# Kernel tuning notes

Measured on AMD Instinct MI355X. Metric: run time of the kernel, lower is better.

The kernel has to match this reference:

```python
import jax, jax.numpy as jnp
from jax import lax
import numpy as np

MS = 128            # local_map_size
HALF = MS // 2
B, S = 8, 64
C, H, W = 3, 1024, 1024


def setup_inputs() -> dict:
    key = jax.random.key(0)
    ks = jax.random.split(key, 48)
    r = lambda i, shape, s: jax.random.normal(ks[i], shape, jnp.float32) * s
    z = lambda *shape: jnp.zeros(shape, jnp.float32)
    o = lambda *shape: jnp.ones(shape, jnp.float32)
    return {
        "full_map": jax.random.normal(ks[0], (B, C, H, W), jnp.float32),
        "conditions": jax.random.uniform(ks[1], (B, 5), jnp.float32, 0.0, 1024.0),
        "input_seq": jax.random.uniform(ks[2], (B, S, 2), jnp.float32, 0.0, 1024.0),
        "steps_remaining": jax.random.uniform(ks[3], (B, S), jnp.float32, 0.0, 500.0),
        # LocalMapEncoder convs (OIHW) + batchnorm affine params
        "cw1": r(4, (16, 3, 3, 3), 0.2),   "cb1": z(16),  "g1": o(16),  "be1": z(16),
        "cw2": r(5, (32, 16, 3, 3), 0.1),  "cb2": z(32),  "g2": o(32),  "be2": z(32),
        "cw3": r(6, (64, 32, 3, 3), 0.07), "cb3": z(64),  "g3": o(64),  "be3": z(64),
        "cw4": r(7, (128, 64, 3, 3), 0.05),"cb4": z(128), "g4": o(128), "be4": z(128),
        "fw1": r(8, (512, 128 * 8 * 8), 0.01), "fb1": z(512),
        "fw2": r(9, (256, 512), 0.04),         "fb2": z(256),
        # ConditionEncoder (6 -> 128 -> 64)
        "ew1": r(10, (128, 6), 0.05),  "eb1": z(128),
        "ew2": r(11, (64, 128), 0.05), "eb2": z(64),
        # coord embedder (2 -> 32)
        "mw": r(12, (32, 2), 0.05), "mb": z(32),
        # 2-layer LSTM, torch gate order (i, f, g, o)
        "w_ih0": r(13, (4 * 256, 32), 0.05),  "w_hh0": r(14, (4 * 256, 256), 0.05),
        "b_ih0": z(4 * 256), "b_hh0": z(4 * 256),
        "w_ih1": r(15, (4 * 256, 256), 0.05), "w_hh1": r(16, (4 * 256, 256), 0.05),
        "b_ih1": z(4 * 256), "b_hh1": z(4 * 256),
        # context layer (256+256+64=576 -> 128 -> 64) and output (64 -> 2)
        "xw1": r(17, (128, 576), 0.04), "xb1": z(128),
        "xw2": r(18, (64, 128), 0.05),  "xb2": z(64),
        "ow": r(19, (2, 64), 0.1),      "ob": z(2),
    }


def _conv_bn_relu(x, w, b, g, be):
    # stride-2 3x3 conv, padding 1, NCHW/OIHW; BatchNorm in training mode (batch stats)
    y = lax.conv_general_dilated(x, w, (2, 2), ((1, 1), (1, 1)),
                                 dimension_numbers=("NCHW", "OIHW", "NCHW"))
    y = y + b[None, :, None, None]
    mu = y.mean((0, 2, 3), keepdims=True)
    var = y.var((0, 2, 3), keepdims=True)
    y = (y - mu) * lax.rsqrt(var + 1e-5) * g[None, :, None, None] + be[None, :, None, None]
    return jax.nn.relu(y)


def _lstm_layer(x, w_ih, w_hh, b_ih, b_hh):
    # x: [B, S, D] -> hidden states [B, S, Hd]
    bsz, hd = x.shape[0], w_hh.shape[1]
    bias = b_ih + b_hh
    def step(carry, xt):
        h, c = carry
        zg = xt @ w_ih.T + h @ w_hh.T + bias
        i, f, gg, oo = jnp.split(zg, 4, axis=-1)
        c = jax.nn.sigmoid(f) * c + jax.nn.sigmoid(i) * jnp.tanh(gg)
        h = jax.nn.sigmoid(oo) * jnp.tanh(c)
        return (h, c), h
    h0 = jnp.zeros((bsz, hd), x.dtype)
    _, hs = lax.scan(step, (h0, h0), x.transpose(1, 0, 2))
    return hs.transpose(1, 0, 2)


def reference(full_map, conditions, input_seq, steps_remaining,
              cw1, cb1, g1, be1, cw2, cb2, g2, be2,
              cw3, cb3, g3, be3, cw4, cb4, g4, be4,
              fw1, fb1, fw2, fb2, ew1, eb1, ew2, eb2, mw, mb,
              w_ih0, w_hh0, b_ih0, b_hh0, w_ih1, w_hh1, b_ih1, b_hh1,
              xw1, xb1, xw2, xb2, ow, ob):
    bsz, seq, _ = input_seq.shape
    # --- batched crop+pad gather (replaces host numpy loop): zero-pad map by
    # HALF on each side, then every crop is a dynamic_slice of size MS at (y, x).
    padded = jnp.pad(full_map, ((0, 0), (0, 0), (HALF, HALF), (HALF, HALF)))
    ys = input_seq[..., 0].astype(jnp.int32).reshape(-1)
    xs = input_seq[..., 1].astype(jnp.int32).reshape(-1)
    bidx = jnp.repeat(jnp.arange(bsz, dtype=jnp.int32), seq)
    crop_one = lambda b, y, x: lax.dynamic_slice(padded, (b, 0, y, x), (1, C, MS, MS))[0]
    crops = jax.vmap(crop_one)(bidx, ys, xs)              # [B*S, C, MS, MS]
    # --- LocalMapEncoder
    h = _conv_bn_relu(crops, cw1, cb1, g1, be1)
    h = _conv_bn_relu(h, cw2, cb2, g2, be2)
    h = _conv_bn_relu(h, cw3, cb3, g3, be3)
    h = _conv_bn_relu(h, cw4, cb4, g4, be4)               # [B*S, 128, 8, 8]
    h = h.reshape(h.shape[0], -1)
    h = jax.nn.relu(h @ fw1.T + fb1) @ fw2.T + fb2
    map_features = h.reshape(bsz, seq, -1)                # [B, S, 256]
    # --- ConditionEncoder on [conditions ++ steps_remaining]
    enh = jnp.concatenate(
        [jnp.broadcast_to(conditions[:, None, :], (bsz, seq, 5)),
         steps_remaining[..., None]], axis=-1)            # [B, S, 6]
    cond_features = jax.nn.relu(enh @ ew1.T + eb1) @ ew2.T + eb2  # [B, S, 64]
    # --- route predictor
    emb = jax.nn.relu(input_seq @ mw.T + mb)              # [B, S, 32]
    lstm_out = _lstm_layer(emb, w_ih0, w_hh0, b_ih0, b_hh0)
    lstm_out = _lstm_layer(lstm_out, w_ih1, w_hh1, b_ih1, b_hh1)  # [B, S, 256]
    combined = jnp.concatenate([lstm_out, map_features, cond_features], axis=-1)
    ctx = jax.nn.relu(jax.nn.relu(combined @ xw1.T + xb1) @ xw2.T + xb2)
    return ctx @ ow.T + ob                                # [B, S, 2]
```

## Files before the change

kernel.cpp:

```cpp
#include <hip/hip_runtime.h>

#define TPB 256
#define NLB 64

typedef float f32x4 __attribute__((ext_vector_type(4)));
typedef short bf16x8 __attribute__((ext_vector_type(8)));
typedef unsigned long long u64;

__device__ __forceinline__ float bf2f(unsigned short u) {
  union { unsigned int i; float f; } x; x.i = ((unsigned int)u) << 16; return x.f;
}
__device__ __forceinline__ unsigned short f2bf(float v) {
  union { float f; unsigned int i; } x; x.f = v;
  unsigned int r = (x.i + 0x7fffu + ((x.i >> 16) & 1u)) >> 16;
  return (unsigned short)r;
}
__device__ __forceinline__ float sigf(float x) { return 1.f / (1.f + __expf(-x)); }
__device__ __forceinline__ bf16x8 lda_bf8(const unsigned short* p) {
  union { uint4 u; bf16x8 v; } t; t.u = *(const uint4*)p; return t.v;
}
__device__ __forceinline__ float fma8(uint4 q, const float* w, float a) {
  union { unsigned int u; float f; } t;
  t.u = q.x << 16;         a = fmaf(w[0], t.f, a);
  t.u = q.x & 0xffff0000u; a = fmaf(w[1], t.f, a);
  t.u = q.y << 16;         a = fmaf(w[2], t.f, a);
  t.u = q.y & 0xffff0000u; a = fmaf(w[3], t.f, a);
  t.u = q.z << 16;         a = fmaf(w[4], t.f, a);
  t.u = q.z & 0xffff0000u; a = fmaf(w[5], t.f, a);
  t.u = q.w << 16;         a = fmaf(w[6], t.f, a);
  t.u = q.w & 0xffff0000u; a = fmaf(w[7], t.f, a);
  return a;
}

__global__ __launch_bounds__(TPB, 2) void conv1_tap(
    const float* __restrict__ fmap, const float* __restrict__ iseq,
    const unsigned short* __restrict__ wT,
    const float* __restrict__ bias,
    unsigned short* __restrict__ out) {
  __shared__ float patch[3][17][132];
  __shared__ unsigned short Bsm[16][104];
  __shared__ float bs[16];
  const int tid = threadIdx.x;
  const int n = blockIdx.x >> 3, R0 = (blockIdx.x & 7) << 3;
  const int y = (int)iseq[n * 2], x = (int)iseq[n * 2 + 1];
  const int bimg = n >> 6;

  for (int e = tid; e < 1536; e += TPB) Bsm[e / 96][e % 96] = wT[e];
  if (tid < 16) bs[tid] = bias[tid];
  for (int e = tid; e < 3 * 17 * 132; e += TPB) {
    int ic = e / 2244, rem = e % 2244, l = rem / 132, c = rem % 132;
    int i = 2 * R0 - 1 + l, j = c - 1;
    float v = 0.f;
    if ((unsigned)i < 128u && (unsigned)j < 128u) {
      int r = y + i - 64, cc = x + j - 64;
      if ((unsigned)r < 1024u && (unsigned)cc < 1024u)
        v = fmap[(((size_t)bimg * 3 + ic) << 20) + ((size_t)r << 10) + cc];
    }
    patch[ic][l][c] = v;
  }
  __syncthreads();

  const int w = tid >> 6, lane = tid & 63, fr = lane & 15, kg = lane >> 4;
  f32x4 acc[8];
#pragma unroll
  for (int m = 0; m < 8; ++m) acc[m] = {0.f, 0.f, 0.f, 0.f};

#pragma unroll
  for (int ch = 0; ch < 3; ++ch) {
    int k8 = ch * 4 + kg;
    int ki = (k8 >= 9) ? 0 : ((k8 * 11) >> 5);
    int kj = (k8 >= 9) ? 0 : (k8 - 3 * ki);
    bf16x8 bfr = lda_bf8(&Bsm[fr][k8 * 8]);
#pragma unroll
    for (int m = 0; m < 8; ++m) {
      int p = w * 128 + m * 16 + fr;
      int pr = p >> 6, pc = p & 63;
      int l = 2 * pr + ki, c = 2 * pc + kj;
      bf16x8 af = {(short)f2bf(patch[0][l][c]), (short)f2bf(patch[1][l][c]),
                   (short)f2bf(patch[2][l][c]), 0, 0, 0, 0, 0};
      acc[m] = __builtin_amdgcn_mfma_f32_16x16x32_bf16(af, bfr, acc[m], 0, 0, 0);
    }
  }
  const int rg = lane >> 4;
  float bb = bs[fr];
#pragma unroll
  for (int m = 0; m < 8; ++m) {
#pragma unroll
    for (int r = 0; r < 4; ++r) {
      int p = w * 128 + m * 16 + rg * 4 + r;
      int pr = p >> 6, pc = p & 63;
      out[(((size_t)n * 64 + R0 + pr) * 64 + pc) * 16 + fr] = f2bf(acc[m][r] + bb);
    }
  }
}

template<int CIN, int COUT_BLK, int NSPLIT, int HIN, int HOUT>
__global__ __launch_bounds__(TPB, 2) void conv_tap(
    const unsigned short* __restrict__ inb,
    const float* __restrict__ ss,
    const unsigned short* __restrict__ wT,
    const float* __restrict__ bias,
    unsigned short* __restrict__ out) {
  constexpr int K = CIN * 9;
  constexpr int K8 = K / 8;
  constexpr int NCH = (K8 + 3) / 4;
  constexpr int KPAD = NCH * 32;
  constexpr int BS = KPAD + 8;
  constexpr int CINP = CIN + 8;
  constexpr int ICG_SH = (CIN == 16) ? 1 : (CIN == 32) ? 2 : 3;
  constexpr int TPR = HOUT / 8;
  constexpr int TILES = TPR * TPR;
  constexpr int NT = COUT_BLK / 16;
  constexpr int COUT_TOT = COUT_BLK * NSPLIT;

  __shared__ unsigned short patch[289 * CINP];
  __shared__ unsigned short Bsm[COUT_BLK * BS];
  __shared__ float ssl[CIN * 2];

  const int tid = threadIdx.x;
  const int bid = blockIdx.x;
  const int n = bid / (TILES * NSPLIT);
  const int rem = bid % (TILES * NSPLIT);
  const int tile = rem / NSPLIT;
  const int split = rem % NSPLIT;
  const int TR0 = (tile / TPR) * 8, TC0 = (tile % TPR) * 8;
  const int oc0 = split * COUT_BLK;

  for (int i = tid; i < CIN * 2; i += TPB) ssl[i] = ss[i];
  __syncthreads();

  for (int e = tid; e < 289 * (CIN / 8); e += TPB) {
    int icg = e % (CIN / 8), pix = e / (CIN / 8);
    int row = pix / 17, col = pix % 17;
    int ir = 2 * TR0 - 1 + row, jc = 2 * TC0 - 1 + col;
    uint4 o = {0u, 0u, 0u, 0u};
    if ((unsigned)ir < (unsigned)HIN && (unsigned)jc < (unsigned)HIN) {
      uint4 v = *(const uint4*)&inb[(((size_t)n * HIN + ir) * HIN + jc) * CIN + icg * 8];
      unsigned int d[4] = {v.x, v.y, v.z, v.w};
      unsigned int* op = (unsigned int*)&o;
#pragma unroll
      for (int t = 0; t < 4; ++t) {
        int c = icg * 8 + 2 * t;
        float a = fmaxf(fmaf(bf2f((unsigned short)(d[t] & 0xffff)), ssl[2 * c], ssl[2 * c + 1]), 0.f);
        float b = fmaxf(fmaf(bf2f((unsigned short)(d[t] >> 16)), ssl[2 * c + 2], ssl[2 * c + 3]), 0.f);
        op[t] = (unsigned int)f2bf(a) | ((unsigned int)f2bf(b) << 16);
      }
    }
    *(uint4*)&patch[pix * CINP + icg * 8] = o;
  }
  constexpr int B8 = COUT_BLK * (KPAD / 8);
  for (int e = tid; e < B8; e += TPB) {
    int oc = e / (KPAD / 8), k8i = e % (KPAD / 8);
    uint4 v = {0u, 0u, 0u, 0u};
    if (k8i * 8 < K) v = *(const uint4*)&wT[(size_t)(oc0 + oc) * K + k8i * 8];
    *(uint4*)&Bsm[oc * BS + k8i * 8] = v;
  }
  __syncthreads();

  const int wave = tid >> 6, lane = tid & 63;
  const int fr = lane & 15, kg = lane >> 4;
  const int p = wave * 16 + fr;
  const int pr = p >> 3, pc = p & 7;
  f32x4 acc[NT];
#pragma unroll
  for (int j = 0; j < NT; ++j) acc[j] = {0.f, 0.f, 0.f, 0.f};

#pragma unroll
  for (int ch = 0; ch < NCH; ++ch) {
    int k8 = ch * 4 + kg;
    int tap = k8 >> ICG_SH, icg = k8 & ((1 << ICG_SH) - 1);
    int ki = (tap * 11) >> 5;
    int kj = tap - 3 * ki;
    int addr = ((2 * pr + ki) * 17 + (2 * pc + kj)) * CINP + icg * 8;
    if (tap >= 9) addr = 0;
    bf16x8 af = lda_bf8(&patch[addr]);
#pragma unroll
    for (int j = 0; j < NT; ++j) {
      bf16x8 bfr = lda_bf8(&Bsm[(j * 16 + fr) * BS + ch * 32 + kg * 8]);
      acc[j] = __builtin_amdgcn_mfma_f32_16x16x32_bf16(af, bfr, acc[j], 0, 0, 0);
    }
  }
  const int rg = lane >> 4;
#pragma unroll
  for (int j = 0; j < NT; ++j) {
    int oc = oc0 + j * 16 + fr;
    float bb = bias[oc];
#pragma unroll
    for (int r = 0; r < 4; ++r) {
      int pp = wave * 16 + rg * 4 + r;
      int orow = TR0 + (pp >> 3), ocol = TC0 + (pp & 7);
      out[(((size_t)n * HOUT + orow) * HOUT + ocol) * COUT_TOT + oc] = f2bf(acc[j][r] + bb);
    }
  }
}

__global__ __launch_bounds__(TPB) void prep_wt(
    const float* __restrict__ w1, const float* __restrict__ w2,
    const float* __restrict__ w3, const float* __restrict__ w4,
    unsigned short* __restrict__ wt1, unsigned short* __restrict__ wt2,
    unsigned short* __restrict__ wt3, unsigned short* __restrict__ wt4) {
  int i = blockIdx.x * TPB + threadIdx.x;
  if (i < 1536) {
    int oc = i / 96, k = i % 96;
    int tap = k >> 3, ic = k & 7;
    float v = (tap < 9 && ic < 3) ? w1[(oc * 3 + ic) * 9 + tap] : 0.f;
    wt1[i] = f2bf(v);
  } else if (i < 6144) {
    int j = i - 1536;
    int oc = j / 144, k = j % 144;
    wt2[j] = f2bf(w2[(oc * 16 + (k & 15)) * 9 + (k >> 4)]);
  } else if (i < 24576) {
    int j = i - 6144;
    int oc = j / 288, k = j % 288;
    wt3[j] = f2bf(w3[(oc * 32 + (k & 31)) * 9 + (k >> 5)]);
  } else if (i < 98304) {
    int j = i - 24576;
    int oc = j / 576, k = j % 576;
    wt4[j] = f2bf(w4[(oc * 64 + (k & 63)) * 9 + (k >> 6)]);
  }
}

__global__ __launch_bounds__(TPB) void permute_fw1(const float* __restrict__ in,
    unsigned short* __restrict__ out) {
  __shared__ unsigned short l[128 * 66];
  int n = blockIdx.x;
  for (int e = threadIdx.x; e < 8192; e += TPB) {
    int c = e >> 6, pix = e & 63;
    l[c * 66 + pix] = f2bf(in[(size_t)n * 8192 + e]);
  }
  __syncthreads();
  for (int e = threadIdx.x; e < 8192; e += TPB) {
    int pix = e >> 7, c = e & 127;
    out[(size_t)n * 8192 + e] = l[c * 66 + pix];
  }
}

#define STAT_NB 512
__global__ __launch_bounds__(TPB) void stats_cl2(
    const unsigned short* __restrict__ y, float* __restrict__ part,
    int C, int total_u4) {
  const int tid = threadIdx.x, bid = blockIdx.x;
  const int NQ = C >> 3;
  float s[8], q[8];
#pragma unroll
  for (int j = 0; j < 8; ++j) { s[j] = 0.f; q[j] = 0.f; }
  for (int i = bid * TPB + tid; i < total_u4; i += STAT_NB * TPB) {
    uint4 v = ((const uint4*)y)[i];
    unsigned int d[4] = {v.x, v.y, v.z, v.w};
#pragma unroll
    for (int t = 0; t < 4; ++t) {
      float a = bf2f((unsigned short)(d[t] & 0xffff));
      float b = bf2f((unsigned short)(d[t] >> 16));
      s[2 * t] += a;     q[2 * t] = fmaf(a, a, q[2 * t]);
      s[2 * t + 1] += b; q[2 * t + 1] = fmaf(b, b, q[2 * t + 1]);
    }
  }
  __shared__ float rs[TPB][8];
  __shared__ float rq[TPB][8];
#pragma unroll
  for (int j = 0; j < 8; ++j) { rs[tid][j] = s[j]; rq[tid][j] = q[j]; }
  __syncthreads();
  for (int off = TPB / 2; off >= NQ; off >>= 1) {
    if (tid < off) {
#pragma unroll
      for (int j = 0; j < 8; ++j) { rs[tid][j] += rs[tid + off][j]; rq[tid][j] += rq[tid + off][j]; }
    }
    __syncthreads();
  }
  if (tid < NQ) {
#pragma unroll
    for (int j = 0; j < 8; ++j) {
      int c = tid * 8 + j;
      part[(size_t)bid * 2 * C + 2 * c] = rs[tid][j];
      part[(size_t)bid * 2 * C + 2 * c + 1] = rq[tid][j];
    }
  }
}

__global__ __launch_bounds__(TPB) void stats_final2(const float* __restrict__ part,
    const float* __restrict__ gamma, const float* __restrict__ beta,
    float* __restrict__ ss, float inv_count, int C) {
  int c = blockIdx.x, tid = threadIdx.x;
  float sum = part[(size_t)tid * 2 * C + 2 * c] + part[(size_t)(tid + 256) * 2 * C + 2 * c];
  float sq  = part[(size_t)tid * 2 * C + 2 * c + 1] + part[(size_t)(tid + 256) * 2 * C + 2 * c + 1];
  __shared__ float rs[TPB], rq[TPB];
  rs[tid] = sum; rq[tid] = sq;
  __syncthreads();
  for (int off = TPB / 2; off > 0; off >>= 1) {
    if (tid < off) { rs[tid] += rs[tid + off]; rq[tid] += rq[tid + off]; }
    __syncthreads();
  }
  if (tid == 0) {
    float mean = rs[0] * inv_count;
    float var  = rq[0] * inv_count - mean * mean;
    float rstd = rsqrtf(var + 1e-5f);
    float scl  = gamma[c] * rstd;
    ss[2 * c] = scl;
    ss[2 * c + 1] = beta[c] - mean * scl;
  }
}

__global__ __launch_bounds__(TPB) void bnrelu_cl(const unsigned short* __restrict__ y,
    const float* __restrict__ ss, unsigned short* __restrict__ out) {
  int q = blockIdx.x * TPB + threadIdx.x;
  if (q >= 524288) return;
  int c0 = (q << 3) & 127;
  uint4 v = ((const uint4*)y)[q];
  unsigned int d[4] = {v.x, v.y, v.z, v.w};
  uint4 o;
  unsigned int* op = (unsigned int*)&o;
#pragma unroll
  for (int t = 0; t < 4; ++t) {
    int c = c0 + 2 * t;
    float a = fmaxf(fmaf(bf2f((unsigned short)(d[t] & 0xffff)), ss[2 * c], ss[2 * c + 1]), 0.f);
    float b = fmaxf(fmaf(bf2f((unsigned short)(d[t] >> 16)), ss[2 * c + 2], ss[2 * c + 3]), 0.f);
    op[t] = (unsigned int)f2bf(a) | ((unsigned int)f2bf(b) << 16);
  }
  ((uint4*)out)[q] = o;
}

__global__ __launch_bounds__(TPB, 2) void fc1_mfma(
    const unsigned short* __restrict__ A, const unsigned short* __restrict__ W,
    const float* __restrict__ bias, float* __restrict__ out) {
  __shared__ unsigned short As[64][64];
  __shared__ unsigned short Bs[64][64];
  const int tid = threadIdx.x;
  const int lane = tid & 63, wave = tid >> 6;
  const int wr = (wave >> 1) * 32, wc = (wave & 1) * 32;
  const int bm = blockIdx.y * 64, bn = blockIdx.x * 64;
  f32x4 acc00 = {0.f, 0.f, 0.f, 0.f}, acc01 = acc00, acc10 = acc00, acc11 = acc00;
  const int r0 = tid >> 3, c0 = tid & 7;
  const int fr = lane & 15, kg = lane >> 4;
  for (int kt = 0; kt < 128; ++kt) {
    const int kb = kt * 64;
    uint4 av0 = *(const uint4*)&A[(size_t)(bm + r0) * 8192 + kb + c0 * 8];
    uint4 av1 = *(const uint4*)&A[(size_t)(bm + r0 + 32) * 8192 + kb + c0 * 8];
    uint4 bv0 = *(const uint4*)&W[(size_t)(bn + r0) * 8192 + kb + c0 * 8];
    uint4 bv1 = *(const uint4*)&W[(size_t)(bn + r0 + 32) * 8192 + kb + c0 * 8];
    __syncthreads();
    *(uint4*)&As[r0][(c0 ^ (r0 & 7)) * 8] = av0;
    *(uint4*)&As[r0 + 32][(c0 ^ (r0 & 7)) * 8] = av1;
    *(uint4*)&Bs[r0][(c0 ^ (r0 & 7)) * 8] = bv0;
    *(uint4*)&Bs[r0 + 32][(c0 ^ (r0 & 7)) * 8] = bv1;
    __syncthreads();
#pragma unroll
    for (int ks = 0; ks < 2; ++ks) {
      int ch = ks * 4 + kg;
      int ra0 = wr + fr, ra1 = wr + 16 + fr;
      int rb0 = wc + fr, rb1 = wc + 16 + fr;
      bf16x8 a_0 = lda_bf8(&As[ra0][(ch ^ (ra0 & 7)) * 8]);
      bf16x8 a_1 = lda_bf8(&As[ra1][(ch ^ (ra1 & 7)) * 8]);
      bf16x8 b_0 = lda_bf8(&Bs[rb0][(ch ^ (rb0 & 7)) * 8]);
      bf16x8 b_1 = lda_bf8(&Bs[rb1][(ch ^ (rb1 & 7)) * 8]);
      acc00 = __builtin_amdgcn_mfma_f32_16x16x32_bf16(a_0, b_0, acc00, 0, 0, 0);
      acc01 = __builtin_amdgcn_mfma_f32_16x16x32_bf16(a_0, b_1, acc01, 0, 0, 0);
      acc10 = __builtin_amdgcn_mfma_f32_16x16x32_bf16(a_1, b_0, acc10, 0, 0, 0);
      acc11 = __builtin_amdgcn_mfma_f32_16x16x32_bf16(a_1, b_1, acc11, 0, 0, 0);
    }
  }
  const int rg = lane >> 4;
  int n0 = bn + wc + fr, n1 = n0 + 16;
  float bi0 = bias[n0], bi1 = bias[n1];
#pragma unroll
  for (int r = 0; r < 4; ++r) {
    int m0 = bm + wr + rg * 4 + r, m1 = m0 + 16;
    out[m0 * 512 + n0] = fmaxf(acc00[r] + bi0, 0.f);
    out[m0 * 512 + n1] = fmaxf(acc01[r] + bi1, 0.f);
    out[m1 * 512 + n0] = fmaxf(acc10[r] + bi0, 0.f);
    out[m1 * 512 + n1] = fmaxf(acc11[r] + bi1, 0.f);
  }
}

__global__ __launch_bounds__(TPB, 2) void gemm_m64(
    const float* __restrict__ A, const float* __restrict__ W,
    const float* __restrict__ bias, float* __restrict__ out,
    int N, int K, int relu, int ldo, int coff) {
  __shared__ unsigned short As[64 * 40];
  __shared__ unsigned short Bs[64 * 40];
  const int tid = threadIdx.x, lane = tid & 63, wave = tid >> 6;
  const int wr = (wave >> 1) * 32, wc = (wave & 1) * 32;
  const int bm = blockIdx.y * 64, bn = blockIdx.x * 64;
  const int fr = lane & 15, kg = lane >> 4;
  const int sr = tid >> 2, sc = (tid & 3) * 8;
  f32x4 a00 = {0.f, 0.f, 0.f, 0.f}, a01 = a00, a10 = a00, a11 = a00;
  int nch = (K + 31) >> 5;
  for (int ch = 0; ch < nch; ++ch) {
    int kb = ch * 32;
    __syncthreads();
    {
      unsigned short tmp[8];
#pragma unroll
      for (int j = 0; j < 8; ++j) {
        int k = kb + sc + j;
        tmp[j] = (k < K) ? f2bf(A[(size_t)(bm + sr) * K + k]) : (unsigned short)0;
      }
      *(uint4*)&As[sr * 40 + sc] = *(const uint4*)tmp;
      int wrow = bn + sr;
#pragma unroll
      for (int j = 0; j < 8; ++j) {
        int k = kb + sc + j;
        tmp[j] = (wrow < N && k < K) ? f2bf(W[(size_t)wrow * K + k]) : (unsigned short)0;
      }
      *(uint4*)&Bs[sr * 40 + sc] = *(const uint4*)tmp;
    }
    __syncthreads();
    bf16x8 af0 = lda_bf8(&As[(wr + fr) * 40 + kg * 8]);
    bf16x8 af1 = lda_bf8(&As[(wr + 16 + fr) * 40 + kg * 8]);
    bf16x8 bf0 = lda_bf8(&Bs[(wc + fr) * 40 + kg * 8]);
    bf16x8 bf1 = lda_bf8(&Bs[(wc + 16 + fr) * 40 + kg * 8]);
    a00 = __builtin_amdgcn_mfma_f32_16x16x32_bf16(af0, bf0, a00, 0, 0, 0);
    a01 = __builtin_amdgcn_mfma_f32_16x16x32_bf16(af0, bf1, a01, 0, 0, 0);
    a10 = __builtin_amdgcn_mfma_f32_16x16x32_bf16(af1, bf0, a10, 0, 0, 0);
    a11 = __builtin_amdgcn_mfma_f32_16x16x32_bf16(af1, bf1, a11, 0, 0, 0);
  }
  const int rg = lane >> 4;
  int n0 = bn + wc + fr, n1 = n0 + 16;
  float bi0 = (n0 < N) ? bias[n0] : 0.f;
  float bi1 = (n1 < N) ? bias[n1] : 0.f;
#pragma unroll
  for (int r = 0; r < 4; ++r) {
    int m0 = bm + wr + rg * 4 + r, m1 = m0 + 16;
    if (n0 < N) {
      float v = a00[r] + bi0; out[(size_t)m0 * ldo + coff + n0] = relu ? fmaxf(v, 0.f) : v;
      v = a10[r] + bi0;       out[(size_t)m1 * ldo + coff + n0] = relu ? fmaxf(v, 0.f) : v;
    }
    if (n1 < N) {
      float v = a01[r] + bi1; out[(size_t)m0 * ldo + coff + n1] = relu ? fmaxf(v, 0.f) : v;
      v = a11[r] + bi1;       out[(size_t)m1 * ldo + coff + n1] = relu ? fmaxf(v, 0.f) : v;
    }
  }
}

__global__ __launch_bounds__(TPB) void build_enh_kernel(const float* __restrict__ cond,
    const float* __restrict__ steps, float* __restrict__ enh) {
  int i = blockIdx.x * TPB + threadIdx.x;
  if (i >= 512 * 6) return;
  int n = i / 6, k = i % 6;
  int b = n >> 6, s = n & 63;
  enh[i] = (k < 5) ? cond[b * 5 + k] : steps[b * 64 + s];
}

__global__ __launch_bounds__(TPB, 1) void lstm_kernel(
    const float* __restrict__ iseq,
    const float* __restrict__ mw, const float* __restrict__ mb,
    const float* __restrict__ w_ih0, const float* __restrict__ w_hh0,
    const float* __restrict__ b_ih0, const float* __restrict__ b_hh0,
    const float* __restrict__ w_ih1, const float* __restrict__ w_hh1,
    const float* __restrict__ b_ih1, const float* __restrict__ b_hh1,
    u64* __restrict__ h0x, u64* __restrict__ h1x,
    float* __restrict__ comb) {
  const int tid = threadIdx.x;
  const int blkid = blockIdx.x;
  const int u0 = blkid * 4;

  __shared__ float xz[64][8][16];
  __shared__ __align__(16) char reg2[26112];
  __shared__ float bias1s[16];

  float (*embc)[8][32] = (float (*)[8][32])reg2;
  float* mwmb = (float*)(reg2 + 16384);
  unsigned short (*v0s)[256] = (unsigned short (*)[256])reg2;
  unsigned short (*w1h)[256] = (unsigned short (*)[256])(reg2 + 4096);
  float (*part0)[8][16] = (float (*)[8][16])(reg2 + 8192);
  float (*part1)[8][16] = (float (*)[8][16])(reg2 + 16384);
  float (*zg0)[16] = (float (*)[16])(reg2 + 24576);
  float (*zg1)[16] = (float (*)[16])(reg2 + 25088);

  const int r = tid & 15, ks = tid >> 4;
  const int R = (r >> 2) * 256 + u0 + (r & 3);

  float w0reg[16], w1reg[32], wtmp[32];
#pragma unroll
  for (int i = 0; i < 16; ++i) w0reg[i] = w_hh0[R * 256 + ks * 16 + i];
  if (ks < 8) {
#pragma unroll
    for (int i = 0; i < 32; ++i) w1reg[i] = w_ih1[R * 256 + ks * 32 + i];
  } else {
#pragma unroll
    for (int i = 0; i < 32; ++i) w1reg[i] = w_hh1[R * 256 + (ks - 8) * 32 + i];
  }
#pragma unroll
  for (int i = 0; i < 32; ++i) wtmp[i] = w_ih0[R * 32 + i];
  const float bias0r = b_ih0[R] + b_hh0[R];
  if (tid < 16) bias1s[tid] = b_ih1[R] + b_hh1[R];
  if (tid < 96) mwmb[tid] = (tid < 64) ? mw[tid] : mb[tid - 64];
  __syncthreads();

  for (int chunk = 0; chunk < 4; ++chunk) {
    if (tid < 128) {
      int pp = tid >> 3, b = tid & 7;
      int pg = chunk * 16 + pp;
      float s0 = iseq[(b * 64 + pg) * 2 + 0];
      float s1 = iseq[(b * 64 + pg) * 2 + 1];
      for (int k = 0; k < 32; ++k)
        embc[pp][b][k] = fmaxf(fmaf(mwmb[2 * k], s0, fmaf(mwmb[2 * k + 1], s1, mwmb[64 + k])), 0.f);
    }
    __syncthreads();
    {
      int pg = chunk * 16 + ks;
      for (int b = 0; b < 8; ++b) {
        float a = bias0r;
        const float* e = &embc[ks][b][0];
#pragma unroll
        for (int k = 0; k < 32; ++k) a = fmaf(wtmp[k], e[k], a);
        xz[pg][b][r] = a;
      }
    }
    __syncthreads();
  }

  float c0 = 0.f, c1 = 0.f;
  for (int p = 0; p <= 64; ++p) {
    if (p >= 1) {
      const unsigned tag0 = (unsigned)p;
      const u64* s0p = &h0x[(size_t)(p - 1) * 1024 + tid * 4];
      u64 a0, a1, a2, a3;
      for (;;) {
        a0 = __hip_atomic_load(&s0p[0], __ATOMIC_RELAXED, __HIP_MEMORY_SCOPE_AGENT);
        a1 = __hip_atomic_load(&s0p[1], __ATOMIC_RELAXED, __HIP_MEMORY_SCOPE_AGENT);
        a2 = __hip_atomic_load(&s0p[2], __ATOMIC_RELAXED, __HIP_MEMORY_SCOPE_AGENT);
        a3 = __hip_atomic_load(&s0p[3], __ATOMIC_RELAXED, __HIP_MEMORY_SCOPE_AGENT);
        if (((unsigned)(a0 >> 32) == tag0) & ((unsigned)(a1 >> 32) == tag0) &
            ((unsigned)(a2 >> 32) == tag0) & ((unsigned)(a3 >> 32) == tag0)) break;
        __builtin_amdgcn_s_sleep(1);
      }
#pragma unroll
      for (int i = 0; i < 4; ++i) {
        int g = tid * 4 + i;
        int bb = (g & 15) >> 1, ub = (g >> 4) * 4 + (g & 1) * 2;
        u64 va = (i == 0) ? a0 : (i == 1) ? a1 : (i == 2) ? a2 : a3;
        *(unsigned int*)&v0s[bb][ub] = (unsigned int)va;
      }
    } else {
#pragma unroll
      for (int i = 0; i < 4; ++i) ((unsigned int*)v0s)[tid * 4 + i] = 0u;
    }
    __syncthreads();

    if (p < 64) {
#pragma unroll
      for (int b = 0; b < 8; ++b) {
        uint4 q0 = *(const uint4*)&v0s[b][ks * 16];
        uint4 q1 = *(const uint4*)&v0s[b][ks * 16 + 8];
        float a = 0.f;
        a = fma8(q0, &w0reg[0], a);
        a = fma8(q1, &w0reg[8], a);
        part0[ks][b][r] = a;
      }
    }
    __syncthreads();

    if (tid < 128) {
      if (p < 64) {
        int b = tid >> 4, rr = tid & 15;
        float s = xz[p][b][rr];
#pragma unroll
        for (int k2 = 0; k2 < 16; ++k2) s += part0[k2][b][rr];
        zg0[b][rr] = s;
      }
    } else {
      int t2 = tid - 128;
      if (p >= 2) {
        const unsigned tag1 = (unsigned)(p - 1);
        const u64* s1p = &h1x[(size_t)(p - 2) * 1024 + t2 * 8];
        u64 e[8];
        for (;;) {
          bool ok = true;
#pragma unroll
          for (int i = 0; i < 8; ++i) {
            e[i] = __hip_atomic_load(&s1p[i], __ATOMIC_RELAXED, __HIP_MEMORY_SCOPE_AGENT);
            ok &= ((unsigned)(e[i] >> 32) == tag1);
          }
          if (ok) break;
          __builtin_amdgcn_s_sleep(1);
        }
#pragma unroll
        for (int i = 0; i < 8; ++i) {
          int g = t2 * 8 + i;
          int bb = (g & 15) >> 1, ub = (g >> 4) * 4 + (g & 1) * 2;
          *(unsigned int*)&w1h[bb][ub] = (unsigned int)e[i];
        }
      } else {
#pragma unroll
        for (int i = 0; i < 8; ++i) ((unsigned int*)w1h)[t2 * 8 + i] = 0u;
      }
    }
    __syncthreads();

    if (tid < 32 && p < 64) {
      int b = tid >> 2, uu = tid & 3;
      float zi = zg0[b][uu], zf = zg0[b][4 + uu], zgv = zg0[b][8 + uu], zo = zg0[b][12 + uu];
      c0 = sigf(zf) * c0 + sigf(zi) * tanhf(zgv);
      float h = sigf(zo) * tanhf(c0);
      float hp = __shfl_xor(h, 1);
      if (!(uu & 1)) {
        unsigned int d = (unsigned int)f2bf(h) | ((unsigned int)f2bf(hp) << 16);
        u64 v = ((u64)(unsigned)(p + 1) << 32) | d;
        __hip_atomic_store(&h0x[(size_t)p * 1024 + blkid * 16 + b * 2 + (uu >> 1)], v,
                           __ATOMIC_RELAXED, __HIP_MEMORY_SCOPE_AGENT);
      }
    }

    if (p >= 1) {
      const unsigned short* sp = (ks < 8) ? &v0s[0][ks * 32] : &w1h[0][(ks - 8) * 32];
#pragma unroll
      for (int b = 0; b < 8; ++b) {
        const uint4* qp = (const uint4*)(sp + b * 256);
        float a = 0.f;
        a = fma8(qp[0], &w1reg[0], a);
        a = fma8(qp[1], &w1reg[8], a);
        a = fma8(qp[2], &w1reg[16], a);
        a = fma8(qp[3], &w1reg[24], a);
        part1[ks][b][r] = a;
      }
    }
    __syncthreads();

    if (tid >= 128 && p >= 1) {
      int t2 = tid - 128, b = t2 >> 4, rr = t2 & 15;
      float s = bias1s[rr];
#pragma unroll
      for (int k2 = 0; k2 < 16; ++k2) s += part1[k2][b][rr];
      zg1[b][rr] = s;
    }
    __syncthreads();

    if (tid < 32 && p >= 1) {
      int b = tid >> 2, uu = tid & 3;
      float zi = zg1[b][uu], zf = zg1[b][4 + uu], zgv = zg1[b][8 + uu], zo = zg1[b][12 + uu];
      c1 = sigf(zf) * c1 + sigf(zi) * tanhf(zgv);
      float h = sigf(zo) * tanhf(c1);
      comb[(size_t)(b * 64 + (p - 1)) * 576 + u0 + uu] = h;
      float hp = __shfl_xor(h, 1);
      if (!(uu & 1)) {
        unsigned int d = (unsigned int)f2bf(h) | ((unsigned int)f2bf(hp) << 16);
        u64 v = ((u64)(unsigned)p << 32) | d;
        __hip_atomic_store(&h1x[(size_t)(p - 1) * 1024 + blkid * 16 + b * 2 + (uu >> 1)], v,
                           __ATOMIC_RELAXED, __HIP_MEMORY_SCOPE_AGENT);
      }
    }
  }
}

extern "C" void kernel_launch(void* const* d_in, const int* in_sizes, int n_in,
                              void* d_out, int out_size, void* d_ws, size_t ws_size,
                              hipStream_t stream) {
  const float* fmap  = (const float*)d_in[0];
  const float* cond  = (const float*)d_in[1];
  const float* iseq  = (const float*)d_in[2];
  const float* steps = (const float*)d_in[3];
  const float* cw1 = (const float*)d_in[4];  const float* cb1 = (const float*)d_in[5];
  const float* g1  = (const float*)d_in[6];  const float* be1 = (const float*)d_in[7];
  const float* cw2 = (const float*)d_in[8];  const float* cb2 = (const float*)d_in[9];
  const float* g2  = (const float*)d_in[10]; const float* be2 = (const float*)d_in[11];
  const float* cw3 = (const float*)d_in[12]; const float* cb3 = (const float*)d_in[13];
  const float* g3  = (const float*)d_in[14]; const float* be3 = (const float*)d_in[15];
  const float* cw4 = (const float*)d_in[16]; const float* cb4 = (const float*)d_in[17];
  const float* g4  = (const float*)d_in[18]; const float* be4 = (const float*)d_in[19];
  const float* fw1 = (const float*)d_in[20]; const float* fb1 = (const float*)d_in[21];
  const float* fw2 = (const float*)d_in[22]; const float* fb2 = (const float*)d_in[23];
  const float* ew1 = (const float*)d_in[24]; const float* eb1 = (const float*)d_in[25];
  const float* ew2 = (const float*)d_in[26]; const float* eb2 = (const float*)d_in[27];
  const float* mw  = (const float*)d_in[28]; const float* mb  = (const float*)d_in[29];
  const float* w_ih0 = (const float*)d_in[30]; const float* w_hh0 = (const float*)d_in[31];
  const float* b_ih0 = (const float*)d_in[32]; const float* b_hh0 = (const float*)d_in[33];
  const float* w_ih1 = (const float*)d_in[34]; const float* w_hh1 = (const float*)d_in[35];
  const float* b_ih1 = (const float*)d_in[36]; const float* b_hh1 = (const float*)d_in[37];
  const float* xw1 = (const float*)d_in[38]; const float* xb1 = (const float*)d_in[39];
  const float* xw2 = (const float*)d_in[40]; const float* xb2 = (const float*)d_in[41];
  const float* ow  = (const float*)d_in[42]; const float* ob  = (const float*)d_in[43];

  float* ws = (float*)d_ws;
  unsigned short* y1bf  = (unsigned short*)ws;
  unsigned short* y2bf  = (unsigned short*)(ws + 16777216);
  unsigned short* y3bf  = (unsigned short*)(ws + 25165824);
  unsigned short* y4pre = (unsigned short*)(ws + 29360128);
  unsigned short* y4bn  = (unsigned short*)(ws + 31457280);
  unsigned short* fw1bf = (unsigned short*)(ws + 33554432);
  size_t base = 35651584;
  float* part  = ws + base; base += 131072;
  float* ss1   = ws + base; base += 32;
  float* ss2   = ws + base; base += 64;
  float* ss3   = ws + base; base += 128;
  float* ss4   = ws + base; base += 256;
  float* f1    = ws + base; base += 262144;
  float* enh   = ws + base; base += 3072;
  float* ceh   = ws + base; base += 65536;
  u64*   h0x   = (u64*)(ws + base); base += 131072;
  u64*   h1x   = (u64*)(ws + base); base += 131072;
  float* comb  = ws + base; base += 294912;
  float* cx1   = ws + base; base += 65536;
  float* cx2   = ws + base; base += 32768;
  unsigned short* wt1 = (unsigned short*)(ws + base); base += 768;
  unsigned short* wt2 = (unsigned short*)(ws + base); base += 2304;
  unsigned short* wt3 = (unsigned short*)(ws + base); base += 9216;
  unsigned short* wt4 = (unsigned short*)(ws + base); base += 36864;

  prep_wt<<<384, TPB, 0, stream>>>(cw1, cw2, cw3, cw4, wt1, wt2, wt3, wt4);
  permute_fw1<<<512, TPB, 0, stream>>>(fw1, fw1bf);

  conv1_tap<<<4096, TPB, 0, stream>>>(fmap, iseq, wt1, cb1, y1bf);
  stats_cl2<<<STAT_NB, TPB, 0, stream>>>(y1bf, part, 16, 4194304);
  stats_final2<<<16, TPB, 0, stream>>>(part, g1, be1, ss1, 1.f / 2097152.f, 16);
  conv_tap<16, 32, 1, 64, 32><<<8192, TPB, 0, stream>>>(y1bf, ss1, wt2, cb2, y2bf);
  stats_cl2<<<STAT_NB, TPB, 0, stream>>>(y2bf, part, 32, 2097152);
  stats_final2<<<32, TPB, 0, stream>>>(part, g2, be2, ss2, 1.f / 524288.f, 32);
  conv_tap<32, 64, 1, 32, 16><<<2048, TPB, 0, stream>>>(y2bf, ss2, wt3, cb3, y3bf);
  stats_cl2<<<STAT_NB, TPB, 0, stream>>>(y3bf, part, 64, 1048576);
  stats_final2<<<64, TPB, 0, stream>>>(part, g3, be3, ss3, 1.f / 131072.f, 64);
  conv_tap<64, 32, 4, 16, 8><<<2048, TPB, 0, stream>>>(y3bf, ss3, wt4, cb4, y4pre);
  stats_cl2<<<STAT_NB, TPB, 0, stream>>>(y4pre, part, 128, 524288);
  stats_final2<<<128, TPB, 0, stream>>>(part, g4, be4, ss4, 1.f / 32768.f, 128);
  bnrelu_cl<<<2048, TPB, 0, stream>>>(y4pre, ss4, y4bn);

  hipMemsetAsync(h0x, 0, 2 * 64 * 1024 * sizeof(u64), stream);
  lstm_kernel<<<NLB, TPB, 0, stream>>>(iseq, mw, mb,
                                       w_ih0, w_hh0, b_ih0, b_hh0,
                                       w_ih1, w_hh1, b_ih1, b_hh1,
                                       h0x, h1x, comb);

  fc1_mfma<<<dim3(8, 8), TPB, 0, stream>>>(y4bn, fw1bf, fb1, f1);
  gemm_m64<<<dim3(4, 8), TPB, 0, stream>>>(f1, fw2, fb2, comb, 256, 512, 0, 576, 256);

  build_enh_kernel<<<12, TPB, 0, stream>>>(cond, steps, enh);
  gemm_m64<<<dim3(2, 8), TPB, 0, stream>>>(enh, ew1, eb1, ceh, 128, 6, 1, 128, 0);
  gemm_m64<<<dim3(1, 8), TPB, 0, stream>>>(ceh, ew2, eb2, comb, 64, 128, 0, 576, 512);

  gemm_m64<<<dim3(2, 8), TPB, 0, stream>>>(comb, xw1, xb1, cx1, 128, 576, 1, 128, 0);
  gemm_m64<<<dim3(1, 8), TPB, 0, stream>>>(cx1, xw2, xb2, cx2, 64, 128, 1, 64, 0);
  gemm_m64<<<dim3(1, 8), TPB, 0, stream>>>(cx2, ow, ob, (float*)d_out, 2, 64, 0, 2, 0);
}
```

Before: 673.6 us.

## Use MFMA for LSTM recurrences, fuse BN-ReLU into fc1, bf16 channel-interleaved conv1 patch

The LSTM recurrent matvecs drop their scalar FMA partial-sum reductions. Weights are now held as bf16 MFMA fragments, one wave each for w_hh0, w_ih1 and w_hh1, which cuts the number of barriers per timestep. The final BatchNorm+ReLU is applied on the fly while fc1 loads its A tile, which removes a separate kernel and an intermediate buffer. conv1 now stores its input patch as bf16 with the channels interleaved, so each fragment is a single 16-byte LDS load instead of three float reads and conversions. The cost is bf16 rounding of the LSTM weights and recurrent state, which lowers precision.

```diff
diff --git a/kernel.cpp b/kernel.cpp
--- a/kernel.cpp
+++ b/kernel.cpp
@@ -19,17 +19,9 @@
 __device__ __forceinline__ bf16x8 lda_bf8(const unsigned short* p) {
   union { uint4 u; bf16x8 v; } t; t.u = *(const uint4*)p; return t.v;
 }
-__device__ __forceinline__ float fma8(uint4 q, const float* w, float a) {
-  union { unsigned int u; float f; } t;
-  t.u = q.x << 16;         a = fmaf(w[0], t.f, a);
-  t.u = q.x & 0xffff0000u; a = fmaf(w[1], t.f, a);
-  t.u = q.y << 16;         a = fmaf(w[2], t.f, a);
-  t.u = q.y & 0xffff0000u; a = fmaf(w[3], t.f, a);
-  t.u = q.z << 16;         a = fmaf(w[4], t.f, a);
-  t.u = q.z & 0xffff0000u; a = fmaf(w[5], t.f, a);
-  t.u = q.w << 16;         a = fmaf(w[6], t.f, a);
-  t.u = q.w & 0xffff0000u; a = fmaf(w[7], t.f, a);
-  return a;
+__device__ __forceinline__ bf16x8 frag_of(const unsigned int* w) {
+  union { unsigned int u[4]; bf16x8 v; } t;
+  t.u[0] = w[0]; t.u[1] = w[1]; t.u[2] = w[2]; t.u[3] = w[3]; return t.v;
 }
 
 __global__ __launch_bounds__(TPB, 2) void conv1_tap(
@@ -37,7 +29,7 @@
     const unsigned short* __restrict__ wT,
     const float* __restrict__ bias,
     unsigned short* __restrict__ out) {
-  __shared__ float patch[3][17][132];
+  __shared__ __align__(16) unsigned short patch[17][132][8];
   __shared__ unsigned short Bsm[16][104];
   __shared__ float bs[16];
   const int tid = threadIdx.x;
@@ -47,6 +39,9 @@
 
   for (int e = tid; e < 1536; e += TPB) Bsm[e / 96][e % 96] = wT[e];
   if (tid < 16) bs[tid] = bias[tid];
+  for (int e = tid; e < 17 * 132; e += TPB)
+    *(uint4*)&patch[e / 132][e % 132][0] = uint4{0u, 0u, 0u, 0u};
+  __syncthreads();
   for (int e = tid; e < 3 * 17 * 132; e += TPB) {
     int ic = e / 2244, rem = e % 2244, l = rem / 132, c = rem % 132;
     int i = 2 * R0 - 1 + l, j = c - 1;
@@ -56,7 +51,7 @@
       if ((unsigned)r < 1024u && (unsigned)cc < 1024u)
         v = fmap[(((size_t)bimg * 3 + ic) << 20) + ((size_t)r << 10) + cc];
     }
-    patch[ic][l][c] = v;
+    patch[l][c][ic] = f2bf(v);
   }
   __syncthreads();
 
@@ -75,9 +70,7 @@
     for (int m = 0; m < 8; ++m) {
       int p = w * 128 + m * 16 + fr;
       int pr = p >> 6, pc = p & 63;
-      int l = 2 * pr + ki, c = 2 * pc + kj;
-      bf16x8 af = {(short)f2bf(patch[0][l][c]), (short)f2bf(patch[1][l][c]),
-                   (short)f2bf(patch[2][l][c]), 0, 0, 0, 0, 0};
+      bf16x8 af = lda_bf8(&patch[2 * pr + ki][2 * pc + kj][0]);
       acc[m] = __builtin_amdgcn_mfma_f32_16x16x32_bf16(af, bfr, acc[m], 0, 0, 0);
     }
   }
@@ -300,30 +293,25 @@
   }
 }
 
-__global__ __launch_bounds__(TPB) void bnrelu_cl(const unsigned short* __restrict__ y,
-    const float* __restrict__ ss, unsigned short* __restrict__ out) {
-  int q = blockIdx.x * TPB + threadIdx.x;
-  if (q >= 524288) return;
-  int c0 = (q << 3) & 127;
-  uint4 v = ((const uint4*)y)[q];
+__device__ __forceinline__ uint4 bnpack(uint4 v, const float* sst) {
   unsigned int d[4] = {v.x, v.y, v.z, v.w};
-  uint4 o;
-  unsigned int* op = (unsigned int*)&o;
+  uint4 o; unsigned int* op = (unsigned int*)&o;
 #pragma unroll
   for (int t = 0; t < 4; ++t) {
-    int c = c0 + 2 * t;
-    float a = fmaxf(fmaf(bf2f((unsigned short)(d[t] & 0xffff)), ss[2 * c], ss[2 * c + 1]), 0.f);
-    float b = fmaxf(fmaf(bf2f((unsigned short)(d[t] >> 16)), ss[2 * c + 2], ss[2 * c + 3]), 0.f);
+    float a = fmaxf(fmaf(bf2f((unsigned short)(d[t] & 0xffff)), sst[4 * t], sst[4 * t + 1]), 0.f);
+    float b = fmaxf(fmaf(bf2f((unsigned short)(d[t] >> 16)), sst[4 * t + 2], sst[4 * t + 3]), 0.f);
     op[t] = (unsigned int)f2bf(a) | ((unsigned int)f2bf(b) << 16);
   }
-  ((uint4*)out)[q] = o;
+  return o;
 }
 
 __global__ __launch_bounds__(TPB, 2) void fc1_mfma(
     const unsigned short* __restrict__ A, const unsigned short* __restrict__ W,
-    const float* __restrict__ bias, float* __restrict__ out) {
+    const float* __restrict__ ss, const float* __restrict__ bias,
+    float* __restrict__ out) {
   __shared__ unsigned short As[64][64];
   __shared__ unsigned short Bs[64][64];
+  __shared__ float ssl[256];
   const int tid = threadIdx.x;
   const int lane = tid & 63, wave = tid >> 6;
   const int wr = (wave >> 1) * 32, wc = (wave & 1) * 32;
@@ -331,13 +319,18 @@
   f32x4 acc00 = {0.f, 0.f, 0.f, 0.f}, acc01 = acc00, acc10 = acc00, acc11 = acc00;
   const int r0 = tid >> 3, c0 = tid & 7;
   const int fr = lane & 15, kg = lane >> 4;
+  for (int i = tid; i < 256; i += TPB) ssl[i] = ss[i];
+  __syncthreads();
   for (int kt = 0; kt < 128; ++kt) {
     const int kb = kt * 64;
     uint4 av0 = *(const uint4*)&A[(size_t)(bm + r0) * 8192 + kb + c0 * 8];
     uint4 av1 = *(const uint4*)&A[(size_t)(bm + r0 + 32) * 8192 + kb + c0 * 8];
     uint4 bv0 = *(const uint4*)&W[(size_t)(bn + r0) * 8192 + kb + c0 * 8];
     uint4 bv1 = *(const uint4*)&W[(size_t)(bn + r0 + 32) * 8192 + kb + c0 * 8];
-    __syncthreads();
+    const float* sst = &ssl[2 * ((kb + c0 * 8) & 127)];
+    __syncthreads();
+    av0 = bnpack(av0, sst);
+    av1 = bnpack(av1, sst);
     *(uint4*)&As[r0][(c0 ^ (r0 & 7)) * 8] = av0;
     *(uint4*)&As[r0 + 32][(c0 ^ (r0 & 7)) * 8] = av1;
     *(uint4*)&Bs[r0][(c0 ^ (r0 & 7)) * 8] = bv0;
@@ -454,31 +447,35 @@
   const int u0 = blkid * 4;
 
   __shared__ float xz[64][8][16];
-  __shared__ __align__(16) char reg2[26112];
+  __shared__ __align__(16) char reg2[18944];
   __shared__ float bias1s[16];
 
   float (*embc)[8][32] = (float (*)[8][32])reg2;
   float* mwmb = (float*)(reg2 + 16384);
-  unsigned short (*v0s)[256] = (unsigned short (*)[256])reg2;
-  unsigned short (*w1h)[256] = (unsigned short (*)[256])(reg2 + 4096);
-  float (*part0)[8][16] = (float (*)[8][16])(reg2 + 8192);
-  float (*part1)[8][16] = (float (*)[8][16])(reg2 + 16384);
-  float (*zg0)[16] = (float (*)[16])(reg2 + 24576);
-  float (*zg1)[16] = (float (*)[16])(reg2 + 25088);
-
+  unsigned short (*v0s)[264] = (unsigned short (*)[264])reg2;
+  unsigned short (*w1h)[264] = (unsigned short (*)[264])(reg2 + 8448);
+  float (*P0)[16]  = (float (*)[16])(reg2 + 16896);
+  float (*P1a)[16] = (float (*)[16])(reg2 + 17408);
+  float (*P1b)[16] = (float (*)[16])(reg2 + 17920);
+
+  const int wv = tid >> 6, lane = tid & 63, fr = lane & 15, kg = lane >> 4;
   const int r = tid & 15, ks = tid >> 4;
-  const int R = (r >> 2) * 256 + u0 + (r & 3);
-
-  float w0reg[16], w1reg[32], wtmp[32];
-#pragma unroll
-  for (int i = 0; i < 16; ++i) w0reg[i] = w_hh0[R * 256 + ks * 16 + i];
-  if (ks < 8) {
-#pragma unroll
-    for (int i = 0; i < 32; ++i) w1reg[i] = w_ih1[R * 256 + ks * 32 + i];
-  } else {
-#pragma unroll
-    for (int i = 0; i < 32; ++i) w1reg[i] = w_hh1[R * 256 + (ks - 8) * 32 + i];
-  }
+  const int R  = (r >> 2) * 256 + u0 + (r & 3);
+  const int Rf = (fr >> 2) * 256 + u0 + (fr & 3);
+
+  unsigned int wfrag[8][4];
+  {
+    const float* wsrc = (wv == 0) ? w_hh0 : (wv == 1) ? w_ih1 : w_hh1;
+#pragma unroll
+    for (int ch = 0; ch < 8; ++ch)
+#pragma unroll
+      for (int d = 0; d < 4; ++d) {
+        float lo = wsrc[(size_t)Rf * 256 + ch * 32 + kg * 8 + d * 2];
+        float hi = wsrc[(size_t)Rf * 256 + ch * 32 + kg * 8 + d * 2 + 1];
+        wfrag[ch][d] = (unsigned)f2bf(lo) | ((unsigned)f2bf(hi) << 16);
+      }
+  }
+  float wtmp[32];
 #pragma unroll
   for (int i = 0; i < 32; ++i) wtmp[i] = w_ih0[R * 32 + i];
   const float bias0r = b_ih0[R] + b_hh0[R];
@@ -509,54 +506,42 @@
     __syncthreads();
   }
 
+  for (int i = tid; i < 8 * 264; i += TPB) {
+    v0s[8 + i / 264][i % 264] = 0;
+    w1h[8 + i / 264][i % 264] = 0;
+  }
+  __syncthreads();
+
   float c0 = 0.f, c1 = 0.f;
   for (int p = 0; p <= 64; ++p) {
-    if (p >= 1) {
-      const unsigned tag0 = (unsigned)p;
-      const u64* s0p = &h0x[(size_t)(p - 1) * 1024 + tid * 4];
-      u64 a0, a1, a2, a3;
-      for (;;) {
-        a0 = __hip_atomic_load(&s0p[0], __ATOMIC_RELAXED, __HIP_MEMORY_SCOPE_AGENT);
-        a1 = __hip_atomic_load(&s0p[1], __ATOMIC_RELAXED, __HIP_MEMORY_SCOPE_AGENT);
-        a2 = __hip_atomic_load(&s0p[2], __ATOMIC_RELAXED, __HIP_MEMORY_SCOPE_AGENT);
-        a3 = __hip_atomic_load(&s0p[3], __ATOMIC_RELAXED, __HIP_MEMORY_SCOPE_AGENT);
-        if (((unsigned)(a0 >> 32) == tag0) & ((unsigned)(a1 >> 32) == tag0) &
-            ((unsigned)(a2 >> 32) == tag0) & ((unsigned)(a3 >> 32) == tag0)) break;
-        __builtin_amdgcn_s_sleep(1);
-      }
-#pragma unroll
-      for (int i = 0; i < 4; ++i) {
-        int g = tid * 4 + i;
-        int bb = (g & 15) >> 1, ub = (g >> 4) * 4 + (g & 1) * 2;
-        u64 va = (i == 0) ? a0 : (i == 1) ? a1 : (i == 2) ? a2 : a3;
-        *(unsigned int*)&v0s[bb][ub] = (unsigned int)va;
-      }
-    } else {
-#pragma unroll
-      for (int i = 0; i < 4; ++i) ((unsigned int*)v0s)[tid * 4 + i] = 0u;
-    }
-    __syncthreads();
-
-    if (p < 64) {
-#pragma unroll
-      for (int b = 0; b < 8; ++b) {
-        uint4 q0 = *(const uint4*)&v0s[b][ks * 16];
-        uint4 q1 = *(const uint4*)&v0s[b][ks * 16 + 8];
-        float a = 0.f;
-        a = fma8(q0, &w0reg[0], a);
-        a = fma8(q1, &w0reg[8], a);
-        part0[ks][b][r] = a;
-      }
-    }
-    __syncthreads();
-
     if (tid < 128) {
-      if (p < 64) {
-        int b = tid >> 4, rr = tid & 15;
-        float s = xz[p][b][rr];
-#pragma unroll
-        for (int k2 = 0; k2 < 16; ++k2) s += part0[k2][b][rr];
-        zg0[b][rr] = s;
+      if (p >= 1) {
+        const unsigned tag0 = (unsigned)p;
+        const u64* s0p = &h0x[(size_t)(p - 1) * 1024 + tid * 8];
+        u64 e[8];
+        for (;;) {
+          bool ok = true;
+#pragma unroll
+          for (int i = 0; i < 8; ++i) {
+            e[i] = __hip_atomic_load(&s0p[i], __ATOMIC_RELAXED, __HIP_MEMORY_SCOPE_AGENT);
+            ok &= ((unsigned)(e[i] >> 32) == tag0);
+          }
+          if (ok) break;
+          __builtin_amdgcn_s_sleep(1);
+        }
+#pragma unroll
+        for (int i = 0; i < 8; ++i) {
+          int g = tid * 8 + i;
+          int bb = (g >> 1) & 7, ub = (g >> 4) * 4 + (g & 1) * 2;
+          *(unsigned int*)&v0s[bb][ub] = (unsigned int)e[i];
+        }
+      } else {
+#pragma unroll
+        for (int i = 0; i < 8; ++i) {
+          int g = tid * 8 + i;
+          int bb = (g >> 1) & 7, ub = (g >> 4) * 4 + (g & 1) * 2;
+          *(unsigned int*)&v0s[bb][ub] = 0u;
+        }
       }
     } else {
       int t2 = tid - 128;
@@ -577,20 +562,72 @@
 #pragma unroll
         for (int i = 0; i < 8; ++i) {
           int g = t2 * 8 + i;
-          int bb = (g & 15) >> 1, ub = (g >> 4) * 4 + (g & 1) * 2;
+          int bb = (g >> 1) & 7, ub = (g >> 4) * 4 + (g & 1) * 2;
           *(unsigned int*)&w1h[bb][ub] = (unsigned int)e[i];
         }
       } else {
 #pragma unroll
-        for (int i = 0; i < 8; ++i) ((unsigned int*)w1h)[t2 * 8 + i] = 0u;
+        for (int i = 0; i < 8; ++i) {
+          int g = t2 * 8 + i;
+          int bb = (g >> 1) & 7, ub = (g >> 4) * 4 + (g & 1) * 2;
+          *(unsigned int*)&w1h[bb][ub] = 0u;
+        }
+      }
+    }
+    __syncthreads();
+
+    if (wv == 0) {
+      if (p < 64) {
+        f32x4 acc = {0.f, 0.f, 0.f, 0.f};
+#pragma unroll
+        for (int ch = 0; ch < 8; ++ch) {
+          bf16x8 af = lda_bf8(&v0s[fr][ch * 32 + kg * 8]);
+          acc = __builtin_amdgcn_mfma_f32_16x16x32_bf16(af, frag_of(wfrag[ch]), acc, 0, 0, 0);
+        }
+#pragma unroll
+        for (int j = 0; j < 4; ++j) {
+          int bb2 = (lane >> 4) * 4 + j;
+          if (bb2 < 8) P0[bb2][fr] = acc[j];
+        }
+      }
+    } else if (wv == 1) {
+      if (p >= 1) {
+        f32x4 acc = {0.f, 0.f, 0.f, 0.f};
+#pragma unroll
+        for (int ch = 0; ch < 8; ++ch) {
+          bf16x8 af = lda_bf8(&v0s[fr][ch * 32 + kg * 8]);
+          acc = __builtin_amdgcn_mfma_f32_16x16x32_bf16(af, frag_of(wfrag[ch]), acc, 0, 0, 0);
+        }
+#pragma unroll
+        for (int j = 0; j < 4; ++j) {
+          int bb2 = (lane >> 4) * 4 + j;
+          if (bb2 < 8) P1a[bb2][fr] = acc[j];
+        }
+      }
+    } else if (wv == 2) {
+      if (p >= 1) {
+        f32x4 acc = {0.f, 0.f, 0.f, 0.f};
+#pragma unroll
+        for (int ch = 0; ch < 8; ++ch) {
+          bf16x8 af = lda_bf8(&w1h[fr][ch * 32 + kg * 8]);
+          acc = __builtin_amdgcn_mfma_f32_16x16x32_bf16(af, frag_of(wfrag[ch]), acc, 0, 0, 0);
+        }
+#pragma unroll
+        for (int j = 0; j < 4; ++j) {
+          int bb2 = (lane >> 4) * 4 + j;
+          if (bb2 < 8) P1b[bb2][fr] = acc[j];
+        }
       }
     }
     __syncthreads();
 
     if (tid < 32 && p < 64) {
       int b = tid >> 2, uu = tid & 3;
-      float zi = zg0[b][uu], zf = zg0[b][4 + uu], zgv = zg0[b][8 + uu], zo = zg0[b][12 + uu];
-      c0 = sigf(zf) * c0 + sigf(zi) * tanhf(zgv);
+      float zi = P0[b][uu]      + xz[p][b][uu];
+      float zf = P0[b][4 + uu]  + xz[p][b][4 + uu];
+      float zg = P0[b][8 + uu]  + xz[p][b][8 + uu];
+      float zo = P0[b][12 + uu] + xz[p][b][12 + uu];
+      c0 = sigf(zf) * c0 + sigf(zi) * tanhf(zg);
       float h = sigf(zo) * tanhf(c0);
       float hp = __shfl_xor(h, 1);
       if (!(uu & 1)) {
@@ -599,36 +636,13 @@
         __hip_atomic_store(&h0x[(size_t)p * 1024 + blkid * 16 + b * 2 + (uu >> 1)], v,
                            __ATOMIC_RELAXED, __HIP_MEMORY_SCOPE_AGENT);
       }
-    }
-
-    if (p >= 1) {
-      const unsigned short* sp = (ks < 8) ? &v0s[0][ks * 32] : &w1h[0][(ks - 8) * 32];
-#pragma unroll
-      for (int b = 0; b < 8; ++b) {
-        const uint4* qp = (const uint4*)(sp + b * 256);
-        float a = 0.f;
-        a = fma8(qp[0], &w1reg[0], a);
-        a = fma8(qp[1], &w1reg[8], a);
-        a = fma8(qp[2], &w1reg[16], a);
-        a = fma8(qp[3], &w1reg[24], a);
-        part1[ks][b][r] = a;
-      }
-    }
-    __syncthreads();
-
-    if (tid >= 128 && p >= 1) {
-      int t2 = tid - 128, b = t2 >> 4, rr = t2 & 15;
-      float s = bias1s[rr];
-#pragma unroll
-      for (int k2 = 0; k2 < 16; ++k2) s += part1[k2][b][rr];
-      zg1[b][rr] = s;
-    }
-    __syncthreads();
-
-    if (tid < 32 && p >= 1) {
-      int b = tid >> 2, uu = tid & 3;
-      float zi = zg1[b][uu], zf = zg1[b][4 + uu], zgv = zg1[b][8 + uu], zo = zg1[b][12 + uu];
-      c1 = sigf(zf) * c1 + sigf(zi) * tanhf(zgv);
+    } else if (tid >= 32 && tid < 64 && p >= 1) {
+      int t2 = tid - 32, b = t2 >> 2, uu = t2 & 3;
+      float zi = P1a[b][uu]      + P1b[b][uu]      + bias1s[uu];
+      float zf = P1a[b][4 + uu]  + P1b[b][4 + uu]  + bias1s[4 + uu];
+      float zg = P1a[b][8 + uu]  + P1b[b][8 + uu]  + bias1s[8 + uu];
+      float zo = P1a[b][12 + uu] + P1b[b][12 + uu] + bias1s[12 + uu];
+      c1 = sigf(zf) * c1 + sigf(zi) * tanhf(zg);
       float h = sigf(zo) * tanhf(c1);
       comb[(size_t)(b * 64 + (p - 1)) * 576 + u0 + uu] = h;
       float hp = __shfl_xor(h, 1);
@@ -675,7 +689,6 @@
   unsigned short* y2bf  = (unsigned short*)(ws + 16777216);
   unsigned short* y3bf  = (unsigned short*)(ws + 25165824);
   unsigned short* y4pre = (unsigned short*)(ws + 29360128);
-  unsigned short* y4bn  = (unsigned short*)(ws + 31457280);
   unsigned short* fw1bf = (unsigned short*)(ws + 33554432);
   size_t base = 35651584;
   float* part  = ws + base; base += 131072;
@@ -711,7 +724,6 @@
   conv_tap<64, 32, 4, 16, 8><<<2048, TPB, 0, stream>>>(y3bf, ss3, wt4, cb4, y4pre);
   stats_cl2<<<STAT_NB, TPB, 0, stream>>>(y4pre, part, 128, 524288);
   stats_final2<<<128, TPB, 0, stream>>>(part, g4, be4, ss4, 1.f / 32768.f, 128);
-  bnrelu_cl<<<2048, TPB, 0, stream>>>(y4pre, ss4, y4bn);
 
   hipMemsetAsync(h0x, 0, 2 * 64 * 1024 * sizeof(u64), stream);
   lstm_kernel<<<NLB, TPB, 0, stream>>>(iseq, mw, mb,
@@ -719,7 +731,7 @@
                                        w_ih1, w_hh1, b_ih1, b_hh1,
                                        h0x, h1x, comb);
 
-  fc1_mfma<<<dim3(8, 8), TPB, 0, stream>>>(y4bn, fw1bf, fb1, f1);
+  fc1_mfma<<<dim3(8, 8), TPB, 0, stream>>>(y4pre, fw1bf, ss4, fb1, f1);
   gemm_m64<<<dim3(4, 8), TPB, 0, stream>>>(f1, fw2, fb2, comb, 256, 512, 0, 576, 256);
 
   build_enh_kernel<<<12, TPB, 0, stream>>>(cond, steps, enh);
```

Result: no change. 670.0 us (-0.5%).
